# Kernel optimization log

Measured on AMD Instinct MI355X. Metric: run time of the kernel, lower is better.

The kernel has to match this reference:

```python
import jax, jax.numpy as jnp
import numpy as np

HIDDEN_DIM = 2048
NUM_HEADS = 16
HEAD_DIM = HIDDEN_DIM // NUM_HEADS


def setup_inputs() -> dict:
    key = jax.random.key(0)
    ks = jax.random.split(key, 5)
    B, S, D = 1, 2048, HIDDEN_DIM
    scale = 1.0 / np.sqrt(D)
    return {
        "x": jax.random.normal(ks[0], (B, S, D), dtype=jnp.float32),
        "w_q": jax.random.normal(ks[1], (D, D), dtype=jnp.float32) * scale,
        "w_k": jax.random.normal(ks[2], (D, D), dtype=jnp.float32) * scale,
        "w_v": jax.random.normal(ks[3], (D, D), dtype=jnp.float32) * scale,
        "w_o": jax.random.normal(ks[4], (D, D), dtype=jnp.float32) * scale,
    }


def reference(x, w_q, w_k, w_v, w_o):
    # x: (B, S, D). Projections use x @ W.T as in the torch module.
    B, S, D = x.shape
    H, Hd = NUM_HEADS, HEAD_DIM
    q = (x @ w_q.T).reshape(B, S, H, Hd)
    k = (x @ w_k.T).reshape(B, S, H, Hd)
    v = (x @ w_v.T).reshape(B, S, H, Hd)
    scale = 1.0 / np.sqrt(Hd).astype(np.float32)
    # The tiled online-softmax loop computes exact softmax attention.
    scores = jnp.einsum("bqhd,bkhd->bhqk", q, k) * scale  # (B,H,S,S)
    p = jax.nn.softmax(scores, axis=-1)
    o = jnp.einsum("bhqk,bkhd->bqhd", p, v).reshape(B, S, D)
    return o @ w_o.T
```

## Files before the change

### kernel.cpp

```cpp
#include <hip/hip_runtime.h>
#include <hip/hip_bf16.h>
#include <cstdint>
#include <cstddef>

typedef __bf16 bf16x8 __attribute__((ext_vector_type(8)));
typedef float f32x4 __attribute__((ext_vector_type(4)));
typedef float f32x16 __attribute__((ext_vector_type(16)));
typedef unsigned short u16x8 __attribute__((ext_vector_type(8)));
typedef unsigned short u16x4 __attribute__((ext_vector_type(4)));

#define S_LEN 2048
#define DMODEL 2048
#define NHEADS 16
#define HD 128

__device__ inline unsigned short f2bf(float f) {
  union { float f; unsigned int u; } v; v.f = f;
  unsigned int r = (v.u + 0x7fffu + ((v.u >> 16) & 1u)) >> 16;
  return (unsigned short)r;
}

__device__ __forceinline__ void gload16(const unsigned short* g,
                                        unsigned short* lds) {
  __builtin_amdgcn_global_load_lds(
      (const __attribute__((address_space(1))) void*)g,
      (__attribute__((address_space(3))) void*)lds, 16, 0, 0);
}

__global__ void cast_all(const float* __restrict__ x, const float* __restrict__ wq,
                         const float* __restrict__ wk, const float* __restrict__ wv,
                         const float* __restrict__ wo,
                         unsigned short* __restrict__ out, float qscale) {
  const int b = blockIdx.x;
  const int seg = b >> 12;
  const int i = ((b & 4095) * 256 + threadIdx.x) * 4;
  const float* src = seg == 0 ? x : seg == 1 ? wq : seg == 2 ? wk
                   : seg == 3 ? wv : wo;
  const float scale = (seg == 1) ? qscale : 1.0f;
  unsigned short* dst = out + (size_t)seg * ((size_t)S_LEN * DMODEL);
  float4 v = *(const float4*)(src + i);
  u16x4 o;
  o.x = f2bf(v.x * scale); o.y = f2bf(v.y * scale);
  o.z = f2bf(v.z * scale); o.w = f2bf(v.w * scale);
  *(u16x4*)(dst + i) = o;
}

template <int MODE>
__device__ __forceinline__ void gemm_core64(
    const unsigned short* __restrict__ A, const unsigned short* __restrict__ B,
    unsigned short* __restrict__ Cb,
    int M, int N, int K, int m0, int n0,
    unsigned short* As, unsigned short* Bs) {
  constexpr int BK = 64;
  const int tid = threadIdx.x;
  const int wave = tid >> 6, lane = tid & 63;
  const int lg = lane >> 4, lr = lane & 15;
  const int rw = (wave >> 1) * 64;
  const int cw = (wave & 1) * 64;
  const int swz = lr & 7;

  const unsigned short* Ap[4];
  const unsigned short* Bp[4];
  unsigned short *as[4], *bs[4];
#pragma unroll
  for (int j = 0; j < 4; j++) {
    const int cc = j * 256 + tid;
    const int row = cc >> 3;
    const int col8 = (cc & 7) ^ (row & 7);
    Ap[j] = A + (size_t)(m0 + row) * K + col8 * 8;
    Bp[j] = B + (size_t)(n0 + row) * K + col8 * 8;
    as[j] = As + j * 2048 + wave * 512;
    bs[j] = Bs + j * 2048 + wave * 512;
  }

  f32x4 acc[4][4];
#pragma unroll
  for (int i = 0; i < 4; i++)
#pragma unroll
    for (int j = 0; j < 4; j++) acc[i][j] = (f32x4){0.f, 0.f, 0.f, 0.f};

  const int nk = K / BK;
  for (int kt = 0; kt < nk; ++kt) {
    const int ko = kt * BK;
    __syncthreads();
#pragma unroll
    for (int j = 0; j < 4; j++) {
      gload16(Ap[j] + ko, as[j]);
      gload16(Bp[j] + ko, bs[j]);
    }
    __syncthreads();

#pragma unroll
    for (int kk = 0; kk < 2; kk++) {
      bf16x8 af[4], bfr[4];
#pragma unroll
      for (int mt = 0; mt < 4; mt++)
        af[mt] = *(const bf16x8*)(As + (rw + mt * 16 + lr) * 64 +
                                  (((kk * 4 + lg) ^ swz) * 8));
#pragma unroll
      for (int nt = 0; nt < 4; nt++)
        bfr[nt] = *(const bf16x8*)(Bs + (cw + nt * 16 + lr) * 64 +
                                   (((kk * 4 + lg) ^ swz) * 8));
#pragma unroll
      for (int mt = 0; mt < 4; mt++)
#pragma unroll
        for (int nt = 0; nt < 4; nt++)
          acc[mt][nt] = __builtin_amdgcn_mfma_f32_16x16x32_bf16(
              af[mt], bfr[nt], acc[mt][nt], 0, 0, 0);
    }
  }

#pragma unroll
  for (int mt = 0; mt < 4; mt++)
#pragma unroll
    for (int nt = 0; nt < 4; nt++) {
      const int col = n0 + cw + nt * 16 + lr;
#pragma unroll
      for (int r = 0; r < 4; r++) {
        const int row = m0 + rw + mt * 16 + lg * 4 + r;
        const float v = acc[mt][nt][r];
        if (MODE == 1) Cb[(size_t)row * N + col] = f2bf(v);
        else Cb[(size_t)col * M + row] = f2bf(v);
      }
    }
}

__global__ __launch_bounds__(256, 3) void gemm_qkv(
    const unsigned short* __restrict__ xb, const unsigned short* __restrict__ wqb,
    const unsigned short* __restrict__ wkb, const unsigned short* __restrict__ wvb,
    unsigned short* __restrict__ qb, unsigned short* __restrict__ kb,
    unsigned short* __restrict__ vTb) {
  __shared__ unsigned short As[128 * 64];
  __shared__ unsigned short Bs[128 * 64];
  const int which = blockIdx.x >> 4;
  const int n0 = (blockIdx.x & 15) * 128;
  const int m0 = blockIdx.y * 128;
  if (which == 0)
    gemm_core64<1>(xb, wqb, qb, S_LEN, DMODEL, DMODEL, m0, n0, As, Bs);
  else if (which == 1)
    gemm_core64<1>(xb, wkb, kb, S_LEN, DMODEL, DMODEL, m0, n0, As, Bs);
  else
    gemm_core64<2>(xb, wvb, vTb, S_LEN, DMODEL, DMODEL, m0, n0, As, Bs);
}

__global__ __launch_bounds__(256, 2) void gemm_bt64(
    const unsigned short* __restrict__ A, const unsigned short* __restrict__ B,
    float* __restrict__ Cf, int M, int N, int K) {
  constexpr int BK = 128;
  __shared__ unsigned short As[64 * 128];
  __shared__ unsigned short Bs[128 * 128];
  const int tid = threadIdx.x;
  const int wave = tid >> 6, lane = tid & 63;
  const int lg = lane >> 4, lr = lane & 15;
  const int rw = (wave >> 1) * 32;
  const int cw = (wave & 1) * 64;
  const int m0 = blockIdx.y * 64, n0 = blockIdx.x * 128;
  const int swz = lr & 7;

  const unsigned short* Ap[4];
  const unsigned short* Bp[8];
  unsigned short *as[4], *bs[8];
#pragma unroll
  for (int j = 0; j < 4; j++) {
    const int cc = j * 256 + tid;
    const int row = cc >> 4;
    const int col16 = (cc & 15) ^ (row & 7);
    Ap[j] = A + (size_t)(m0 + row) * K + col16 * 8;
    as[j] = As + j * 2048 + wave * 512;
  }
#pragma unroll
  for (int j = 0; j < 8; j++) {
    const int cc = j * 256 + tid;
    const int row = cc >> 4;
    const int col16 = (cc & 15) ^ (row & 7);
    Bp[j] = B + (size_t)(n0 + row) * K + col16 * 8;
    bs[j] = Bs + j * 2048 + wave * 512;
  }

  f32x4 acc[2][4];
#pragma unroll
  for (int i = 0; i < 2; i++)
#pragma unroll
    for (int j = 0; j < 4; j++) acc[i][j] = (f32x4){0.f, 0.f, 0.f, 0.f};

  const int nk = K / BK;
  for (int kt = 0; kt < nk; ++kt) {
    const int ko = kt * BK;
    __syncthreads();
#pragma unroll
    for (int j = 0; j < 4; j++) gload16(Ap[j] + ko, as[j]);
#pragma unroll
    for (int j = 0; j < 8; j++) gload16(Bp[j] + ko, bs[j]);
    __syncthreads();

#pragma unroll
    for (int kk = 0; kk < 4; kk++) {
      bf16x8 af[2], bfr[4];
#pragma unroll
      for (int mt = 0; mt < 2; mt++)
        af[mt] = *(const bf16x8*)(As + (rw + mt * 16 + lr) * 128 +
                                  (((kk * 4 + lg) ^ swz) * 8));
#pragma unroll
      for (int nt = 0; nt < 4; nt++)
        bfr[nt] = *(const bf16x8*)(Bs + (cw + nt * 16 + lr) * 128 +
                                   (((kk * 4 + lg) ^ swz) * 8));
#pragma unroll
      for (int mt = 0; mt < 2; mt++)
#pragma unroll
        for (int nt = 0; nt < 4; nt++)
          acc[mt][nt] = __builtin_amdgcn_mfma_f32_16x16x32_bf16(
              af[mt], bfr[nt], acc[mt][nt], 0, 0, 0);
    }
  }

#pragma unroll
  for (int mt = 0; mt < 2; mt++)
#pragma unroll
    for (int nt = 0; nt < 4; nt++) {
      const int col = n0 + cw + nt * 16 + lr;
#pragma unroll
      for (int r = 0; r < 4; r++) {
        const int row = m0 + rw + mt * 16 + lg * 4 + r;
        Cf[(size_t)row * N + col] = acc[mt][nt][r];
      }
    }
}

__global__ __launch_bounds__(256, 2) void attn_kernel(
    const unsigned short* __restrict__ q, const unsigned short* __restrict__ k,
    const unsigned short* __restrict__ vT, unsigned short* __restrict__ o) {
  constexpr int KT = 64;
  __shared__ unsigned short Ks[2][64 * 136];
  __shared__ unsigned short Vt[2][128 * 72];
  __shared__ float Lred[4][32];

  const int tid = threadIdx.x;
  const int w = tid >> 6, lane = tid & 63;
  const int l32 = lane & 31, lh = lane >> 5;
  const int qh = w >> 1;
  const int kh = w & 1;
  const int h = blockIdx.y;
  const int q0 = blockIdx.x * 64;

  bf16x8 qf[8];
#pragma unroll
  for (int ks = 0; ks < 8; ks++)
    qf[ks] = *(const bf16x8*)(q + (size_t)(q0 + qh * 32 + l32) * DMODEL +
                              h * HD + ks * 16 + lh * 8);

  f32x16 Oacc[4];
#pragma unroll
  for (int mt = 0; mt < 4; mt++)
#pragma unroll
    for (int j = 0; j < 16; j++) Oacc[mt][j] = 0.f;
  f32x4 lsumv = (f32x4){0.f, 0.f, 0.f, 0.f};

  int krow[4], kcg[4], vrow[4], vcg[4], kso[4], vso[4];
#pragma unroll
  for (int i = 0; i < 4; i++) {
    const int c = i * 256 + tid;
    krow[i] = c >> 4; kcg[i] = c & 15;
    vrow[i] = c >> 3; vcg[i] = c & 7;
    kso[i] = krow[i] * 136 + kcg[i] * 8;
    vso[i] = vrow[i] * 72 + vcg[i] * 8;
  }

  int kfo[8];
#pragma unroll
  for (int ks = 0; ks < 8; ks++)
    kfo[ks] = (kh * 32 + l32) * 136 + (ks * 2 + lh) * 8;
  int vfo[4][2];
#pragma unroll
  for (int mt = 0; mt < 4; mt++)
#pragma unroll
    for (int s = 0; s < 2; s++)
      vfo[mt][s] = (mt * 32 + l32) * 72 + (kh * 4 + s * 2 + lh) * 8;

  u16x8 kreg[4], vreg[4];
#pragma unroll
  for (int i = 0; i < 4; i++) {
    kreg[i] = *(const u16x8*)(k + (size_t)(krow[i]) * DMODEL + h * HD + kcg[i] * 8);
    vreg[i] = *(const u16x8*)(vT + (size_t)(h * HD + vrow[i]) * S_LEN + vcg[i] * 8);
  }
#pragma unroll
  for (int i = 0; i < 4; i++) {
    *(u16x8*)(Ks[0] + kso[i]) = kreg[i];
    *(u16x8*)(Vt[0] + vso[i]) = vreg[i];
  }
  __syncthreads();

  constexpr int NT = S_LEN / KT;
  for (int kt = 0; kt < NT; ++kt) {
    if (kt + 1 < NT) {
      const int kbase = (kt + 1) * KT;
#pragma unroll
      for (int i = 0; i < 4; i++) {
        kreg[i] = *(const u16x8*)(k + (size_t)(kbase + krow[i]) * DMODEL +
                                  h * HD + kcg[i] * 8);
        vreg[i] = *(const u16x8*)(vT + (size_t)(h * HD + vrow[i]) * S_LEN +
                                  kbase + vcg[i] * 8);
      }
    }

    const unsigned short* Kb = Ks[kt & 1];
    f32x16 sacc0, sacc1;
#pragma unroll
    for (int j = 0; j < 16; j++) { sacc0[j] = 0.f; sacc1[j] = 0.f; }
    __builtin_amdgcn_s_setprio(1);
#pragma unroll
    for (int ks = 0; ks < 4; ks++) {
      const bf16x8 kf0 = *(const bf16x8*)(Kb + kfo[ks]);
      const bf16x8 kf1 = *(const bf16x8*)(Kb + kfo[ks + 4]);
      sacc0 = __builtin_amdgcn_mfma_f32_32x32x16_bf16(kf0, qf[ks], sacc0, 0, 0, 0);
      sacc1 = __builtin_amdgcn_mfma_f32_32x32x16_bf16(kf1, qf[ks + 4], sacc1, 0, 0, 0);
    }
    __builtin_amdgcn_s_setprio(0);
    const f32x16 sacc = sacc0 + sacc1;

    float p[16];
#pragma unroll
    for (int r = 0; r < 16; r++) p[r] = __builtin_amdgcn_exp2f(sacc[r]);
#pragma unroll
    for (int r = 0; r < 4; r++)
      lsumv[r] += (p[4 * r] + p[4 * r + 1]) + (p[4 * r + 2] + p[4 * r + 3]);

    unsigned int Aw[8];
#pragma unroll
    for (int i = 0; i < 8; i++)
      asm("v_cvt_pk_bf16_f32 %0, %1, %2"
          : "=v"(Aw[i]) : "v"(p[2 * i]), "v"(p[2 * i + 1]));
    asm volatile("v_permlane32_swap_b32 %0, %1" : "+v"(Aw[0]), "+v"(Aw[2]));
    asm volatile("v_permlane32_swap_b32 %0, %1" : "+v"(Aw[1]), "+v"(Aw[3]));
    asm volatile("v_permlane32_swap_b32 %0, %1" : "+v"(Aw[4]), "+v"(Aw[6]));
    asm volatile("v_permlane32_swap_b32 %0, %1" : "+v"(Aw[5]), "+v"(Aw[7]));
    union { unsigned int wd[4]; bf16x8 v; } u0, u1;
    u0.wd[0] = Aw[0]; u0.wd[1] = Aw[1]; u0.wd[2] = Aw[2]; u0.wd[3] = Aw[3];
    u1.wd[0] = Aw[4]; u1.wd[1] = Aw[5]; u1.wd[2] = Aw[6]; u1.wd[3] = Aw[7];
    const bf16x8 pfr0 = u0.v, pfr1 = u1.v;

    const unsigned short* Vb = Vt[kt & 1];
    __builtin_amdgcn_s_setprio(1);
#pragma unroll
    for (int mt = 0; mt < 4; mt++) {
      const bf16x8 v0 = *(const bf16x8*)(Vb + vfo[mt][0]);
      const bf16x8 v1 = *(const bf16x8*)(Vb + vfo[mt][1]);
      Oacc[mt] = __builtin_amdgcn_mfma_f32_32x32x16_bf16(v0, pfr0, Oacc[mt], 0, 0, 0);
      Oacc[mt] = __builtin_amdgcn_mfma_f32_32x32x16_bf16(v1, pfr1, Oacc[mt], 0, 0, 0);
    }
    __builtin_amdgcn_s_setprio(0);

    if (kt + 1 < NT) {
      unsigned short* Kn = Ks[(kt + 1) & 1];
      unsigned short* Vn = Vt[(kt + 1) & 1];
#pragma unroll
      for (int i = 0; i < 4; i++) {
        *(u16x8*)(Kn + kso[i]) = kreg[i];
        *(u16x8*)(Vn + vso[i]) = vreg[i];
      }
    }
    __syncthreads();
  }

  float lsum = (lsumv[0] + lsumv[1]) + (lsumv[2] + lsumv[3]);
  lsum += __shfl_xor(lsum, 32);
  if (lh == 0) Lred[w][l32] = lsum;

  float* Of = (float*)(&Ks[0][0]);
  if (kh == 1) {
#pragma unroll
    for (int mt = 0; mt < 4; mt++)
#pragma unroll
      for (int r = 0; r < 16; r++)
        Of[qh * 4096 + mt * 1024 + r * 64 + lh * 32 + l32] = Oacc[mt][r];
  }
  __syncthreads();

  unsigned short* Tb = &Vt[0][0];
  if (kh == 0) {
    const float ltot = Lred[qh * 2][l32] + Lred[qh * 2 + 1][l32];
    const float inv = 1.0f / ltot;
#pragma unroll
    for (int mt = 0; mt < 4; mt++)
#pragma unroll
      for (int rq = 0; rq < 4; rq++) {
        u16x4 pk;
#pragma unroll
        for (int ri = 0; ri < 4; ri++) {
          const int r = rq * 4 + ri;
          const float v = Oacc[mt][r] +
              Of[qh * 4096 + mt * 1024 + r * 64 + lh * 32 + l32];
          pk[ri] = f2bf(v * inv);
        }
        *(u16x4*)(Tb + (qh * 32 + l32) * 136 + mt * 32 + rq * 8 + lh * 4) = pk;
      }
  }
  __syncthreads();

#pragma unroll
  for (int i = 0; i < 4; i++) {
    const int c = i * 256 + tid;
    const int row = c >> 4, ch = c & 15;
    const u16x8 vv = *(const u16x8*)(Tb + row * 136 + ch * 8);
    *(u16x8*)(o + (size_t)(q0 + row) * DMODEL + h * HD + ch * 8) = vv;
  }
}

extern "C" void kernel_launch(void* const* d_in, const int* in_sizes, int n_in,
                              void* d_out, int out_size, void* d_ws, size_t ws_size,
                              hipStream_t stream) {
  (void)in_sizes; (void)n_in; (void)out_size; (void)ws_size;
  const float* x  = (const float*)d_in[0];
  const float* wq = (const float*)d_in[1];
  const float* wk = (const float*)d_in[2];
  const float* wv = (const float*)d_in[3];
  const float* wo = (const float*)d_in[4];
  float* out = (float*)d_out;

  const size_t NE = (size_t)S_LEN * DMODEL;
  unsigned short* ws = (unsigned short*)d_ws;
  unsigned short* xb  = ws + 0 * NE;
  unsigned short* wqb = ws + 1 * NE;
  unsigned short* wkb = ws + 2 * NE;
  unsigned short* wvb = ws + 3 * NE;
  unsigned short* wob = ws + 4 * NE;
  unsigned short* qb  = ws + 5 * NE;
  unsigned short* kb  = ws + 6 * NE;
  unsigned short* vTb = ws + 7 * NE;
  unsigned short* ob  = ws + 8 * NE;

  const float qscale = 0.08838834764831845f * 1.4426950408889634f;

  cast_all<<<dim3(5 * 4096), dim3(256), 0, stream>>>(x, wq, wk, wv, wo, ws,
                                                     qscale);

  gemm_qkv<<<dim3(48, 16), dim3(256), 0, stream>>>(xb, wqb, wkb, wvb, qb, kb,
                                                   vTb);

  attn_kernel<<<dim3(S_LEN / 64, NHEADS), dim3(256), 0, stream>>>(qb, kb, vTb,
                                                                  ob);

  gemm_bt64<<<dim3(16, 32), dim3(256), 0, stream>>>(ob, wob, out, S_LEN,
                                                    DMODEL, DMODEL);
}
```

Measured before the change: 243.9 us.

## Load V fragments directly from global, drop V LDS staging, remap blocks to heads

The attention kernel stops staging V tiles through shared memory and has each wave load its V MFMA fragments straight from global (L2) memory every iteration. This removes the V LDS stores, the LDS reads and part of the LDS footprint. The launch-bounds occupancy hint goes from 2 to 3 blocks per CU, and block indices are remapped so neighbouring blocks are spread across heads, which may change L2 locality. The risk is global-load latency landing on the PV MFMA path with no prefetch, plus register pressure from the higher occupancy target.

```diff
diff --git a/kernel.cpp b/kernel.cpp
--- a/kernel.cpp
+++ b/kernel.cpp
@@ -226,12 +226,12 @@
     }
 }
 
-__global__ __launch_bounds__(256, 2) void attn_kernel(
+__global__ __launch_bounds__(256, 3) void attn_kernel(
     const unsigned short* __restrict__ q, const unsigned short* __restrict__ k,
     const unsigned short* __restrict__ vT, unsigned short* __restrict__ o) {
   constexpr int KT = 64;
   __shared__ unsigned short Ks[2][64 * 136];
-  __shared__ unsigned short Vt[2][128 * 72];
+  __shared__ unsigned short Tb[64 * 136];
   __shared__ float Lred[4][32];
 
   const int tid = threadIdx.x;
@@ -239,8 +239,11 @@
   const int l32 = lane & 31, lh = lane >> 5;
   const int qh = w >> 1;
   const int kh = w & 1;
-  const int h = blockIdx.y;
-  const int q0 = blockIdx.x * 64;
+
+  const int b = blockIdx.y * gridDim.x + blockIdx.x;
+  const int slot = b >> 3;
+  const int h = (b & 7) * 2 + (slot >> 5);
+  const int q0 = (slot & 31) * 64;
 
   bf16x8 qf[8];
 #pragma unroll
@@ -255,38 +258,34 @@
     for (int j = 0; j < 16; j++) Oacc[mt][j] = 0.f;
   f32x4 lsumv = (f32x4){0.f, 0.f, 0.f, 0.f};
 
-  int krow[4], kcg[4], vrow[4], vcg[4], kso[4], vso[4];
+  int krow[4], kcg[4], kso[4];
 #pragma unroll
   for (int i = 0; i < 4; i++) {
     const int c = i * 256 + tid;
     krow[i] = c >> 4; kcg[i] = c & 15;
-    vrow[i] = c >> 3; vcg[i] = c & 7;
     kso[i] = krow[i] * 136 + kcg[i] * 8;
-    vso[i] = vrow[i] * 72 + vcg[i] * 8;
   }
 
   int kfo[8];
 #pragma unroll
   for (int ks = 0; ks < 8; ks++)
     kfo[ks] = (kh * 32 + l32) * 136 + (ks * 2 + lh) * 8;
-  int vfo[4][2];
+
+  const unsigned short* vbase = vT + (size_t)h * HD * S_LEN;
+  int vofs[8];
 #pragma unroll
   for (int mt = 0; mt < 4; mt++)
 #pragma unroll
     for (int s = 0; s < 2; s++)
-      vfo[mt][s] = (mt * 32 + l32) * 72 + (kh * 4 + s * 2 + lh) * 8;
-
-  u16x8 kreg[4], vreg[4];
-#pragma unroll
-  for (int i = 0; i < 4; i++) {
+      vofs[mt * 2 + s] = (mt * 32 + l32) * S_LEN + (kh * 4 + s * 2 + lh) * 8;
+
+  u16x8 kreg[4];
+#pragma unroll
+  for (int i = 0; i < 4; i++)
     kreg[i] = *(const u16x8*)(k + (size_t)(krow[i]) * DMODEL + h * HD + kcg[i] * 8);
-    vreg[i] = *(const u16x8*)(vT + (size_t)(h * HD + vrow[i]) * S_LEN + vcg[i] * 8);
-  }
-#pragma unroll
-  for (int i = 0; i < 4; i++) {
+#pragma unroll
+  for (int i = 0; i < 4; i++)
     *(u16x8*)(Ks[0] + kso[i]) = kreg[i];
-    *(u16x8*)(Vt[0] + vso[i]) = vreg[i];
-  }
   __syncthreads();
 
   constexpr int NT = S_LEN / KT;
@@ -294,12 +293,9 @@
     if (kt + 1 < NT) {
       const int kbase = (kt + 1) * KT;
 #pragma unroll
-      for (int i = 0; i < 4; i++) {
+      for (int i = 0; i < 4; i++)
         kreg[i] = *(const u16x8*)(k + (size_t)(kbase + krow[i]) * DMODEL +
                                   h * HD + kcg[i] * 8);
-        vreg[i] = *(const u16x8*)(vT + (size_t)(h * HD + vrow[i]) * S_LEN +
-                                  kbase + vcg[i] * 8);
-      }
     }
 
     const unsigned short* Kb = Ks[kt & 1];
@@ -316,6 +312,11 @@
     }
     __builtin_amdgcn_s_setprio(0);
     const f32x16 sacc = sacc0 + sacc1;
+
+    bf16x8 vfr[8];
+#pragma unroll
+    for (int i = 0; i < 8; i++)
+      vfr[i] = *(const bf16x8*)(vbase + vofs[i] + kt * KT);
 
     float p[16];
 #pragma unroll
@@ -338,25 +339,21 @@
     u1.wd[0] = Aw[4]; u1.wd[1] = Aw[5]; u1.wd[2] = Aw[6]; u1.wd[3] = Aw[7];
     const bf16x8 pfr0 = u0.v, pfr1 = u1.v;
 
-    const unsigned short* Vb = Vt[kt & 1];
     __builtin_amdgcn_s_setprio(1);
 #pragma unroll
     for (int mt = 0; mt < 4; mt++) {
-      const bf16x8 v0 = *(const bf16x8*)(Vb + vfo[mt][0]);
-      const bf16x8 v1 = *(const bf16x8*)(Vb + vfo[mt][1]);
-      Oacc[mt] = __builtin_amdgcn_mfma_f32_32x32x16_bf16(v0, pfr0, Oacc[mt], 0, 0, 0);
-      Oacc[mt] = __builtin_amdgcn_mfma_f32_32x32x16_bf16(v1, pfr1, Oacc[mt], 0, 0, 0);
+      Oacc[mt] = __builtin_amdgcn_mfma_f32_32x32x16_bf16(vfr[mt * 2], pfr0,
+                                                         Oacc[mt], 0, 0, 0);
+      Oacc[mt] = __builtin_amdgcn_mfma_f32_32x32x16_bf16(vfr[mt * 2 + 1], pfr1,
+                                                         Oacc[mt], 0, 0, 0);
     }
     __builtin_amdgcn_s_setprio(0);
 
     if (kt + 1 < NT) {
       unsigned short* Kn = Ks[(kt + 1) & 1];
-      unsigned short* Vn = Vt[(kt + 1) & 1];
-#pragma unroll
-      for (int i = 0; i < 4; i++) {
+#pragma unroll
+      for (int i = 0; i < 4; i++)
         *(u16x8*)(Kn + kso[i]) = kreg[i];
-        *(u16x8*)(Vn + vso[i]) = vreg[i];
-      }
     }
     __syncthreads();
   }
@@ -375,7 +372,6 @@
   }
   __syncthreads();
 
-  unsigned short* Tb = &Vt[0][0];
   if (kh == 0) {
     const float ltot = Lred[qh * 2][l32] + Lred[qh * 2 + 1][l32];
     const float inv = 1.0f / ltot;
```

Result: slower. 372.4 us (+52.7%).
